# Kernel optimization log

Hardware: AMD Instinct MI355X
Metric: run time of the kernel (lower is better)

The kernel has to match this reference:

```python
import jax, jax.numpy as jnp
import numpy as np

B, N, C = 4, 1029, 1024
H = 16           # num_heads
L = 8            # num_blocks
DH = C // H      # head_dim = 64
HID = 4 * C      # mlp hidden
SCALE = DH ** -0.5
EPS = 1e-6


def _ln(x, w, b):
    mu = jnp.mean(x, axis=-1, keepdims=True)
    var = jnp.var(x, axis=-1, keepdims=True)
    return (x - mu) * jax.lax.rsqrt(var + EPS) * w + b


def setup_inputs() -> dict:
    key = jax.random.key(0)
    ks = jax.random.split(key, 16)
    s = 0.02
    return {
        "x": jax.random.normal(ks[0], (B, N, C), dtype=jnp.float32),
        "ln1_w": jnp.ones((L, C), jnp.float32),
        "ln1_b": jnp.zeros((L, C), jnp.float32),
        "qkv_w": jax.random.normal(ks[1], (L, 3 * C, C), jnp.float32) * s,
        "qkv_b": jnp.zeros((L, 3 * C), jnp.float32),
        "proj_w": jax.random.normal(ks[2], (L, C, C), jnp.float32) * s,
        "proj_b": jnp.zeros((L, C), jnp.float32),
        "ln2_w": jnp.ones((L, C), jnp.float32),
        "ln2_b": jnp.zeros((L, C), jnp.float32),
        "fc1_w": jax.random.normal(ks[3], (L, HID, C), jnp.float32) * s,
        "fc1_b": jnp.zeros((L, HID), jnp.float32),
        "fc2_w": jax.random.normal(ks[4], (L, C, HID), jnp.float32) * s,
        "fc2_b": jnp.zeros((L, C), jnp.float32),
        "norm_w": jnp.ones((C,), jnp.float32),
        "norm_b": jnp.zeros((C,), jnp.float32),
    }


def _block(x, p):
    ln1_w, ln1_b, qkv_w, qkv_b, proj_w, proj_b, ln2_w, ln2_b, fc1_w, fc1_b, fc2_w, fc2_b = p
    # --- attention (manual fp32 QK^T / softmax / AV, as in Attention.forward) ---
    h = _ln(x, ln1_w, ln1_b)
    qkv = h @ qkv_w.T + qkv_b                        # [B,N,3C]
    qkv = qkv.reshape(B, N, 3, H, DH).transpose(2, 0, 3, 1, 4)  # [3,B,H,N,DH]
    q, k, v = qkv[0], qkv[1], qkv[2]
    attn = jnp.einsum("bhnd,bhmd->bhnm", q.astype(jnp.float32), k.astype(jnp.float32)) * SCALE
    # original subtracts row max before softmax; jax.nn.softmax is the same stable math
    attn = jax.nn.softmax(attn, axis=-1).astype(v.dtype)
    o = jnp.einsum("bhnm,bhmd->bhnd", attn, v)       # [B,H,N,DH]
    o = o.transpose(0, 2, 1, 3).reshape(B, N, C)
    x = x + (o @ proj_w.T + proj_b)
    # --- MLP (exact GELU, as nn.GELU default) ---
    h = _ln(x, ln2_w, ln2_b)
    h = jax.nn.gelu(h @ fc1_w.T + fc1_b, approximate=False)
    x = x + (h @ fc2_w.T + fc2_b)
    return x


def reference(x, ln1_w, ln1_b, qkv_w, qkv_b, proj_w, proj_b, ln2_w, ln2_b,
              fc1_w, fc1_b, fc2_w, fc2_b, norm_w, norm_b):
    params = (ln1_w, ln1_b, qkv_w, qkv_b, proj_w, proj_b, ln2_w, ln2_b,
              fc1_w, fc1_b, fc2_w, fc2_b)

    def body(h, p):
        return _block(h, p), None

    x, _ = jax.lax.scan(body, x, params)
    return _ln(x, norm_w, norm_b)
```

## Files before the change

kernel.cpp:

```cpp
#include <hip/hip_runtime.h>
#include <cstdint>
#include <cstddef>

#define B_    4
#define N_TOK 1029
#define C_    1024
#define H_    16
#define DH_   64
#define L_    8
#define HID_  4096
#define M_TOK (B_*N_TOK)
#define MP2_  4352
#define GMB_  34
#define KVB_  128
#define KVT2_ 9
#define KPAD_ 1152

typedef float f32x4 __attribute__((ext_vector_type(4)));
typedef short bf16x8 __attribute__((ext_vector_type(8)));

__device__ __forceinline__ uint16_t f2bf(float f) {
  uint32_t u = __float_as_uint(f);
  u += 0x7fffu + ((u >> 16) & 1u);
  return (uint16_t)(u >> 16);
}

__device__ __forceinline__ void async_copy16(const uint16_t* src, uint16_t* lds_dst) {
  __builtin_amdgcn_global_load_lds(
      (const __attribute__((address_space(1))) void*)src,
      (__attribute__((address_space(3))) void*)lds_dst, 16, 0, 0);
}

__device__ __forceinline__ int swz16(int row, int byte_in_row) {
  return row * 128 + (byte_in_row ^ ((row & 7) << 4));
}


__global__ __launch_bounds__(256)
void cvt_packB(const float* __restrict__ in, uint16_t* __restrict__ out,
               int K, int logsteps, int matsize) {
  const int lyr = blockIdx.y;
  const int t = blockIdx.x * 256 + threadIdx.x;
  const int lane = t & 63;
  const int j = (t >> 6) & 3;
  const int kk = (t >> 8) & ((1 << logsteps) - 1);
  const int pn = t >> (8 + logsteps);
  const int n = pn * 64 + j * 16 + (lane & 15);
  const int k0 = (kk << 5) + (lane >> 4) * 8;
  const float* src = in + (size_t)lyr * matsize + (size_t)n * K + k0;
  const float4 v0 = *(const float4*)(src);
  const float4 v1 = *(const float4*)(src + 4);
  uint64_t p0 = (uint64_t)f2bf(v0.x) | ((uint64_t)f2bf(v0.y) << 16)
              | ((uint64_t)f2bf(v0.z) << 32) | ((uint64_t)f2bf(v0.w) << 48);
  uint64_t p1 = (uint64_t)f2bf(v1.x) | ((uint64_t)f2bf(v1.y) << 16)
              | ((uint64_t)f2bf(v1.z) << 32) | ((uint64_t)f2bf(v1.w) << 48);
  uint64_t* dst = (uint64_t*)(out + (size_t)lyr * matsize + (size_t)t * 8);
  dst[0] = p0; dst[1] = p1;
}

template<int OUTMODE>
__global__ __launch_bounds__(256)
void ln_fwd(const float* __restrict__ x, const float* __restrict__ w,
            const float* __restrict__ b, void* __restrict__ outp) {
  const int row = blockIdx.x;
  const int tid = threadIdx.x;
  const float4 v = reinterpret_cast<const float4*>(x + (size_t)row * C_)[tid];
  float s  = v.x + v.y + v.z + v.w;
  float s2 = v.x*v.x + v.y*v.y + v.z*v.z + v.w*v.w;
  #pragma unroll
  for (int d = 1; d < 64; d <<= 1) {
    s  += __shfl_xor(s, d);
    s2 += __shfl_xor(s2, d);
  }
  __shared__ float red[8];
  const int wv = tid >> 6;
  if ((tid & 63) == 0) { red[wv] = s; red[wv + 4] = s2; }
  __syncthreads();
  s  = red[0] + red[1] + red[2] + red[3];
  s2 = red[4] + red[5] + red[6] + red[7];
  const float mu = s * (1.0f / C_);
  const float rs = rsqrtf(fmaxf(s2 * (1.0f / C_) - mu * mu, 0.0f) + 1e-6f);
  const float4 wv4 = reinterpret_cast<const float4*>(w)[tid];
  const float4 bv4 = reinterpret_cast<const float4*>(b)[tid];
  const float o0 = (v.x - mu) * rs * wv4.x + bv4.x;
  const float o1 = (v.y - mu) * rs * wv4.y + bv4.y;
  const float o2 = (v.z - mu) * rs * wv4.z + bv4.z;
  const float o3 = (v.w - mu) * rs * wv4.w + bv4.w;
  if (OUTMODE == 2) {
    const int c0 = tid * 4;
    const int kk = c0 >> 5, l4p = (c0 >> 3) & 3, e0 = c0 & 7;
    const int pm = row >> 6, ii = (row >> 4) & 3;
    const int lanep = l4p * 16 + (row & 15);
    const uint64_t pk = (uint64_t)f2bf(o0) | ((uint64_t)f2bf(o1) << 16)
                      | ((uint64_t)f2bf(o2) << 32) | ((uint64_t)f2bf(o3) << 48);
    uint16_t* op = (uint16_t*)outp;
    *(uint64_t*)(op + ((((size_t)pm * 32 + kk) * 4 + ii) * 64 + lanep) * 8 + e0) = pk;
  } else {
    float4 o; o.x = o0; o.y = o1; o.z = o2; o.w = o3;
    reinterpret_cast<float4*>((float*)outp + (size_t)row * C_)[tid] = o;
  }
}

template<int EPI, int SPLIT>
__global__ __launch_bounds__(256, 3)
void gemm_reg(const uint16_t* __restrict__ Apk, const uint16_t* __restrict__ Bpk,
              const float* __restrict__ bias, uint16_t* __restrict__ outb,
              float* __restrict__ pbuf, int Nn, int K, int outKsteps,
              uint16_t* __restrict__ Qp, uint16_t* __restrict__ Kp,
              uint16_t* __restrict__ VTp) {
  const int nwg = (int)gridDim.x;
  const int q8 = nwg >> 3, r8 = nwg & 7;
  const int xcd = (int)blockIdx.x & 7, pos = (int)blockIdx.x >> 3;
  const int wgid = (xcd < r8 ? xcd * (q8 + 1) : r8 * (q8 + 1) + (xcd - r8) * q8) + pos;
  const int NB = Nn >> 7;
  const int kc  = (SPLIT > 1) ? wgid / (GMB_ * NB) : 0;
  const int rem = (SPLIT > 1) ? wgid % (GMB_ * NB) : wgid;
  const int bn = rem / GMB_, bm = rem % GMB_;

  const int tid = (int)threadIdx.x;
  const int l = tid & 63, w = tid >> 6;
  const int l15 = l & 15, l4 = l >> 4;
  const int wr = w >> 1, wc = w & 1;
  const int steps = K >> 5;
  const int kcsteps = steps / SPLIT;

  const uint16_t* Aw = Apk + ((size_t)(bm * 2 + wr) * steps + (size_t)kc * kcsteps) * 2048 + l * 8;
  const uint16_t* Bw = Bpk + ((size_t)(bn * 2 + wc) * steps + (size_t)kc * kcsteps) * 2048 + l * 8;

  f32x4 acc[4][4] = {};
  bf16x8 a0[4], b0[4], a1[4], b1[4];

  auto ld0 = [&](int s) {
    const uint16_t* ap = Aw + (size_t)s * 2048;
    const uint16_t* bp = Bw + (size_t)s * 2048;
    #pragma unroll
    for (int i = 0; i < 4; ++i) a0[i] = *(const bf16x8*)(ap + i * 512);
    #pragma unroll
    for (int j = 0; j < 4; ++j) b0[j] = *(const bf16x8*)(bp + j * 512);
  };
  auto ld1 = [&](int s) {
    const uint16_t* ap = Aw + (size_t)s * 2048;
    const uint16_t* bp = Bw + (size_t)s * 2048;
    #pragma unroll
    for (int i = 0; i < 4; ++i) a1[i] = *(const bf16x8*)(ap + i * 512);
    #pragma unroll
    for (int j = 0; j < 4; ++j) b1[j] = *(const bf16x8*)(bp + j * 512);
  };
  auto mm0 = [&] {
    #pragma unroll
    for (int i = 0; i < 4; ++i)
      #pragma unroll
      for (int j = 0; j < 4; ++j)
        acc[i][j] = __builtin_amdgcn_mfma_f32_16x16x32_bf16(a0[i], b0[j], acc[i][j], 0, 0, 0);
  };
  auto mm1 = [&] {
    #pragma unroll
    for (int i = 0; i < 4; ++i)
      #pragma unroll
      for (int j = 0; j < 4; ++j)
        acc[i][j] = __builtin_amdgcn_mfma_f32_16x16x32_bf16(a1[i], b1[j], acc[i][j], 0, 0, 0);
  };

  ld0(0);
  for (int s = 0; s + 2 <= kcsteps; s += 2) {
    ld1(s + 1);
    mm0();
    if (s + 2 < kcsteps) ld0(s + 2);
    mm1();
  }

  #pragma unroll
  for (int j = 0; j < 4; ++j) {
    const int col = bn * 128 + wc * 64 + j * 16 + l15;
    const float bv = (EPI == 3) ? 0.0f : bias[col];
    #pragma unroll
    for (int i = 0; i < 4; ++i) {
      const int mb = bm * 128 + wr * 64 + i * 16 + l4 * 4;
      #pragma unroll
      for (int r = 0; r < 4; ++r) {
        const int m = mb + r;
        const float v = acc[i][j][r] + bv;
        if (EPI == 1) {
          const float u = -1.5957691216f * (v + 0.044715f * v * v * v);
          const float g = v * __builtin_amdgcn_rcpf(1.0f + __expf(u));
          const int pm = m >> 6, ii = (m >> 4) & 3;
          const int kk = col >> 5, l4p = (col >> 3) & 3, e = col & 7;
          const int lanep = l4p * 16 + (m & 15);
          outb[((((size_t)pm * outKsteps + kk) * 4 + ii) * 64 + lanep) * 8 + e] = f2bf(g);
        } else if (EPI == 3) {
          pbuf[((size_t)kc * MP2_ + m) * C_ + col] = v;
        } else {
          if (m < M_TOK) {
            const int which = col >> 10;
            const int h = (col >> 6) & 15;
            const int d = col & 63;
            const int b = m / N_TOK;
            const int key = m - b * N_TOK;
            const int bh = b * 16 + h;
            if (which == 0)      Qp[((size_t)bh * KPAD_ + key) * 64 + d] = f2bf(v * 0.125f);
            else if (which == 1) Kp[((size_t)bh * KPAD_ + key) * 64 + d] = f2bf(v);
            else                 VTp[((size_t)bh * 64 + d) * KPAD_ + key] = f2bf(v);
          }
        }
      }
    }
  }
}

template<int KCH>
__global__ __launch_bounds__(256)
void reduce_add(const float* __restrict__ pbuf, const float* __restrict__ bias,
                float* __restrict__ xbuf) {
  const int m = blockIdx.x;
  const int c4 = threadIdx.x;
  float4 s = reinterpret_cast<const float4*>(bias)[c4];
  #pragma unroll
  for (int kc = 0; kc < KCH; ++kc) {
    const float4 pv = reinterpret_cast<const float4*>(pbuf + ((size_t)kc * MP2_ + m) * C_)[c4];
    s.x += pv.x; s.y += pv.y; s.z += pv.z; s.w += pv.w;
  }
  float4 x = reinterpret_cast<float4*>(xbuf + (size_t)m * C_)[c4];
  x.x += s.x; x.y += s.y; x.z += s.z; x.w += s.w;
  reinterpret_cast<float4*>(xbuf + (size_t)m * C_)[c4] = x;
}

__global__ __launch_bounds__(256, 3)
void attn_fwd(const uint16_t* __restrict__ Qp, const uint16_t* __restrict__ Kp,
              const uint16_t* __restrict__ VTp, uint16_t* __restrict__ ob) {
  __shared__ uint16_t Ksm_[KVB_ * 64];
  __shared__ uint16_t Vsm_[64 * KVB_];
  __shared__ uint16_t Psm_[4][16 * 136];

  const int tid = (int)threadIdx.x;
  const int l = tid & 63, w = tid >> 6;
  const int l15 = l & 15, l4 = l >> 4;
  const int bh = (int)blockIdx.x;
  const int qt = (int)blockIdx.y;

  const uint16_t* Kb = Kp + (size_t)bh * KPAD_ * 64;
  const uint16_t* Vb = VTp + (size_t)bh * 64 * KPAD_;

  bf16x8 qf[2];
  {
    const int qrow = qt * 64 + w * 16 + l15;
    const uint16_t* qbase = Qp + ((size_t)bh * KPAD_ + qrow) * 64;
    qf[0] = *(const bf16x8*)(qbase + l4 * 8);
    qf[1] = *(const bf16x8*)(qbase + 32 + l4 * 8);
  }

  float mrow = -1e30f, lrow = 0.0f;
  f32x4 oacc[4] = {};

  const int krow_s = tid >> 3;
  const int kslot_s = (tid & 7) ^ (krow_s & 7);
  const int vd_s = tid >> 4;
  const int vslot_s = (tid & 15) ^ (vd_s & 15);

  for (int kt = 0; kt < KVT2_; ++kt) {
    const int key0 = kt * KVB_;
    __syncthreads();
    #pragma unroll
    for (int it = 0; it < 4; ++it) {
      const int row = it * 32 + krow_s;
      async_copy16(Kb + (size_t)(key0 + row) * 64 + kslot_s * 8,
                   Ksm_ + it * 2048 + tid * 8);
    }
    #pragma unroll
    for (int it = 0; it < 4; ++it) {
      const int d = it * 16 + vd_s;
      async_copy16(Vb + (size_t)d * KPAD_ + key0 + vslot_s * 8,
                   Vsm_ + it * 2048 + tid * 8);
    }
    __syncthreads();

    f32x4 s[8];
    #pragma unroll
    for (int kf = 0; kf < 8; ++kf) s[kf] = f32x4{0.f, 0.f, 0.f, 0.f};
    #pragma unroll
    for (int kk = 0; kk < 2; ++kk) {
      #pragma unroll
      for (int kf = 0; kf < 8; ++kf) {
        const bf16x8 kfrag = *(const bf16x8*)((const char*)Ksm_ + swz16(kf * 16 + l15, kk * 64 + l4 * 16));
        s[kf] = __builtin_amdgcn_mfma_f32_16x16x32_bf16(kfrag, qf[kk], s[kf], 0, 0, 0);
      }
    }
    if (kt == KVT2_ - 1) {
      #pragma unroll
      for (int kf = 0; kf < 8; ++kf)
        #pragma unroll
        for (int r = 0; r < 4; ++r)
          if (key0 + kf * 16 + l4 * 4 + r >= N_TOK) s[kf][r] = -1e30f;
    }
    float pmx = s[0][0];
    #pragma unroll
    for (int kf = 0; kf < 8; ++kf)
      #pragma unroll
      for (int r = 0; r < 4; ++r) pmx = fmaxf(pmx, s[kf][r]);
    pmx = fmaxf(pmx, __shfl_xor(pmx, 16));
    pmx = fmaxf(pmx, __shfl_xor(pmx, 32));
    if (!__all(pmx - mrow <= 8.0f)) {
      const float mi = fmaxf(mrow, pmx);
      const float sc = __expf(mrow - mi);
      mrow = mi;
      lrow *= sc;
      #pragma unroll
      for (int df = 0; df < 4; ++df)
        #pragma unroll
        for (int r = 0; r < 4; ++r) oacc[df][r] *= sc;
    }
    float psum = 0.0f;
    #pragma unroll
    for (int kf = 0; kf < 8; ++kf) {
      const float p0 = __expf(s[kf][0] - mrow);
      const float p1 = __expf(s[kf][1] - mrow);
      const float p2 = __expf(s[kf][2] - mrow);
      const float p3 = __expf(s[kf][3] - mrow);
      psum += (p0 + p1) + (p2 + p3);
      const uint64_t pk = (uint64_t)f2bf(p0) | ((uint64_t)f2bf(p1) << 16)
                        | ((uint64_t)f2bf(p2) << 32) | ((uint64_t)f2bf(p3) << 48);
      *(uint64_t*)(&Psm_[w][l15 * 136 + kf * 16 + l4 * 4]) = pk;
    }
    psum += __shfl_xor(psum, 16);
    psum += __shfl_xor(psum, 32);
    lrow += psum;
    #pragma unroll
    for (int kk = 0; kk < 4; ++kk) {
      const bf16x8 pf = *(const bf16x8*)(&Psm_[w][l15 * 136 + kk * 32 + l4 * 8]);
      #pragma unroll
      for (int df = 0; df < 4; ++df) {
        const int d = df * 16 + l15;
        const bf16x8 vfrag = *(const bf16x8*)(Vsm_ + d * KVB_ + (((kk * 4 + l4) ^ (d & 15)) * 8));
        oacc[df] = __builtin_amdgcn_mfma_f32_16x16x32_bf16(vfrag, pf, oacc[df], 0, 0, 0);
      }
    }
  }

  const int q = qt * 64 + w * 16 + l15;
  if (q < N_TOK) {
    const float inv = 1.0f / lrow;
    const int m = (bh >> 4) * N_TOK + q;
    const int pmq = m >> 6, ii = (m >> 4) & 3, m15 = m & 15;
    const int hbase = (bh & 15) * 64;
    #pragma unroll
    for (int df = 0; df < 4; ++df)
      #pragma unroll
      for (int r = 0; r < 4; ++r) {
        const int c = hbase + df * 16 + l4 * 4 + r;
        const int kkp = c >> 5, l4p = (c >> 3) & 3, e = c & 7;
        ob[((((size_t)pmq * 32 + kkp) * 4 + ii) * 64 + l4p * 16 + m15) * 8 + e] =
            f2bf(oacc[df][r] * inv);
      }
  }
}

extern "C" void kernel_launch(void* const* d_in, const int* in_sizes, int n_in,
                              void* d_out, int out_size, void* d_ws, size_t ws_size,
                              hipStream_t stream) {
  const float* x_in   = (const float*)d_in[0];
  const float* ln1_w  = (const float*)d_in[1];
  const float* ln1_b  = (const float*)d_in[2];
  const float* qkv_w  = (const float*)d_in[3];
  const float* qkv_b  = (const float*)d_in[4];
  const float* proj_w = (const float*)d_in[5];
  const float* proj_b = (const float*)d_in[6];
  const float* ln2_w  = (const float*)d_in[7];
  const float* ln2_b  = (const float*)d_in[8];
  const float* fc1_w  = (const float*)d_in[9];
  const float* fc1_b  = (const float*)d_in[10];
  const float* fc2_w  = (const float*)d_in[11];
  const float* fc2_b  = (const float*)d_in[12];
  const float* norm_w = (const float*)d_in[13];
  const float* norm_b = (const float*)d_in[14];

  char* p = (char*)d_ws;
  float*    xbuf = (float*)p;     p += (size_t)MP2_ * C_ * 4;
  uint16_t* hbuf = (uint16_t*)p;  p += (size_t)MP2_ * C_ * 2;
  uint16_t* big  = (uint16_t*)p;  p += (size_t)MP2_ * HID_ * 2;
  uint16_t* wq   = (uint16_t*)p;  p += (size_t)L_ * 3 * C_ * C_ * 2;
  uint16_t* wp   = (uint16_t*)p;  p += (size_t)L_ * C_ * C_ * 2;
  uint16_t* w1   = (uint16_t*)p;  p += (size_t)L_ * HID_ * C_ * 2;
  uint16_t* w2   = (uint16_t*)p;  p += (size_t)L_ * C_ * HID_ * 2;
  uint16_t* qp   = (uint16_t*)p;  p += (size_t)64 * KPAD_ * 64 * 2;
  uint16_t* kp   = (uint16_t*)p;  p += (size_t)64 * KPAD_ * 64 * 2;
  uint16_t* vtp  = (uint16_t*)p;  p += (size_t)64 * 64 * KPAD_ * 2;
  float*    pbuf = (float*)p;     p += (size_t)2 * MP2_ * C_ * 4;
  if ((size_t)(p - (char*)d_ws) > ws_size) return;

  hipMemcpyAsync(xbuf, x_in, (size_t)M_TOK * C_ * sizeof(float),
                 hipMemcpyDeviceToDevice, stream);

  cvt_packB<<<dim3(3 * C_ * C_ / 2048, L_), dim3(256), 0, stream>>>(qkv_w,  wq, C_,   5, 3 * C_ * C_);
  cvt_packB<<<dim3(C_ * C_ / 2048, L_),     dim3(256), 0, stream>>>(proj_w, wp, C_,   5, C_ * C_);
  cvt_packB<<<dim3(HID_ * C_ / 2048, L_),   dim3(256), 0, stream>>>(fc1_w,  w1, C_,   5, HID_ * C_);
  cvt_packB<<<dim3(C_ * HID_ / 2048, L_),   dim3(256), 0, stream>>>(fc2_w,  w2, HID_, 7, C_ * HID_);

  for (int lyr = 0; lyr < L_; ++lyr) {
    ln_fwd<2><<<dim3(M_TOK), dim3(256), 0, stream>>>(
        xbuf, ln1_w + (size_t)lyr * C_, ln1_b + (size_t)lyr * C_, hbuf);
    gemm_reg<4, 1><<<dim3((3 * C_ / 128) * GMB_), dim3(256), 0, stream>>>(
        hbuf, wq + (size_t)lyr * 3 * C_ * C_, qkv_b + (size_t)lyr * 3 * C_,
        nullptr, nullptr, 3 * C_, C_, 0, qp, kp, vtp);
    attn_fwd<<<dim3(64, 17), dim3(256), 0, stream>>>(qp, kp, vtp, hbuf);
    gemm_reg<3, 2><<<dim3(2 * (C_ / 128) * GMB_), dim3(256), 0, stream>>>(
        hbuf, wp + (size_t)lyr * C_ * C_, nullptr,
        nullptr, pbuf, C_, C_, 0, nullptr, nullptr, nullptr);
    reduce_add<2><<<dim3(M_TOK), dim3(256), 0, stream>>>(
        pbuf, proj_b + (size_t)lyr * C_, xbuf);
    ln_fwd<2><<<dim3(M_TOK), dim3(256), 0, stream>>>(
        xbuf, ln2_w + (size_t)lyr * C_, ln2_b + (size_t)lyr * C_, hbuf);
    gemm_reg<1, 1><<<dim3((HID_ / 128) * GMB_), dim3(256), 0, stream>>>(
        hbuf, w1 + (size_t)lyr * HID_ * C_, fc1_b + (size_t)lyr * HID_,
        big, nullptr, HID_, C_, HID_ >> 5, nullptr, nullptr, nullptr);
    gemm_reg<3, 2><<<dim3(2 * (C_ / 128) * GMB_), dim3(256), 0, stream>>>(
        big, w2 + (size_t)lyr * C_ * HID_, nullptr,
        nullptr, pbuf, C_, HID_, 0, nullptr, nullptr, nullptr);
    reduce_add<2><<<dim3(M_TOK), dim3(256), 0, stream>>>(
        pbuf, fc2_b + (size_t)lyr * C_, xbuf);
  }
  ln_fwd<1><<<dim3(M_TOK), dim3(256), 0, stream>>>(xbuf, norm_w, norm_b, d_out);
}
```

Baseline: 2.795 ms.

## Replace register-direct packed GEMM with LDS double-buffered 256x256 tile GEMM

Swaps the old GEMM, which loaded pre-packed bf16 fragments straight into registers, for a 512-thread kernel. The new kernel stages 256x256 tiles of row-major A and W into swizzled LDS with async global-to-LDS copies and double buffering. A separate 256-thread tail path handles the leftover rows beyond 4096. The packed layouts are dropped: weights are converted with a plain elementwise cast, and LN and attention write row-major bf16. The fc2 split-K goes from 2 to 4, which adds reduction traffic in exchange for more workgroups. The larger tiles raise data reuse per workgroup but cut the workgroup count and occupancy, and the tail path is a simple unpipelined loop.

```diff
diff --git a/kernel.cpp b/kernel.cpp
--- a/kernel.cpp
+++ b/kernel.cpp
@@ -6,12 +6,12 @@
 #define N_TOK 1029
 #define C_    1024
 #define H_    16
-#define DH_   64
 #define L_    8
 #define HID_  4096
 #define M_TOK (B_*N_TOK)
 #define MP2_  4352
-#define GMB_  34
+#define TM0_  4096
+#define PROWS 4224
 #define KVB_  128
 #define KVT2_ 9
 #define KPAD_ 1152
@@ -35,27 +35,15 @@
   return row * 128 + (byte_in_row ^ ((row & 7) << 4));
 }
 
-
 __global__ __launch_bounds__(256)
-void cvt_packB(const float* __restrict__ in, uint16_t* __restrict__ out,
-               int K, int logsteps, int matsize) {
-  const int lyr = blockIdx.y;
-  const int t = blockIdx.x * 256 + threadIdx.x;
-  const int lane = t & 63;
-  const int j = (t >> 6) & 3;
-  const int kk = (t >> 8) & ((1 << logsteps) - 1);
-  const int pn = t >> (8 + logsteps);
-  const int n = pn * 64 + j * 16 + (lane & 15);
-  const int k0 = (kk << 5) + (lane >> 4) * 8;
-  const float* src = in + (size_t)lyr * matsize + (size_t)n * K + k0;
-  const float4 v0 = *(const float4*)(src);
-  const float4 v1 = *(const float4*)(src + 4);
-  uint64_t p0 = (uint64_t)f2bf(v0.x) | ((uint64_t)f2bf(v0.y) << 16)
-              | ((uint64_t)f2bf(v0.z) << 32) | ((uint64_t)f2bf(v0.w) << 48);
-  uint64_t p1 = (uint64_t)f2bf(v1.x) | ((uint64_t)f2bf(v1.y) << 16)
-              | ((uint64_t)f2bf(v1.z) << 32) | ((uint64_t)f2bf(v1.w) << 48);
-  uint64_t* dst = (uint64_t*)(out + (size_t)lyr * matsize + (size_t)t * 8);
-  dst[0] = p0; dst[1] = p1;
+void cvt_f32_bf16(const float* __restrict__ in, uint16_t* __restrict__ out, int n4) {
+  int i = blockIdx.x * 256 + threadIdx.x;
+  if (i < n4) {
+    float4 v = reinterpret_cast<const float4*>(in)[i];
+    uint64_t pk = (uint64_t)f2bf(v.x) | ((uint64_t)f2bf(v.y) << 16)
+                | ((uint64_t)f2bf(v.z) << 32) | ((uint64_t)f2bf(v.w) << 48);
+    reinterpret_cast<uint64_t*>(out)[i] = pk;
+  }
 }
 
 template<int OUTMODE>
@@ -86,123 +74,196 @@
   const float o1 = (v.y - mu) * rs * wv4.y + bv4.y;
   const float o2 = (v.z - mu) * rs * wv4.z + bv4.z;
   const float o3 = (v.w - mu) * rs * wv4.w + bv4.w;
-  if (OUTMODE == 2) {
-    const int c0 = tid * 4;
-    const int kk = c0 >> 5, l4p = (c0 >> 3) & 3, e0 = c0 & 7;
-    const int pm = row >> 6, ii = (row >> 4) & 3;
-    const int lanep = l4p * 16 + (row & 15);
-    const uint64_t pk = (uint64_t)f2bf(o0) | ((uint64_t)f2bf(o1) << 16)
-                      | ((uint64_t)f2bf(o2) << 32) | ((uint64_t)f2bf(o3) << 48);
-    uint16_t* op = (uint16_t*)outp;
-    *(uint64_t*)(op + ((((size_t)pm * 32 + kk) * 4 + ii) * 64 + lanep) * 8 + e0) = pk;
+  if (OUTMODE == 0) {
+    uint64_t pk = (uint64_t)f2bf(o0) | ((uint64_t)f2bf(o1) << 16)
+                | ((uint64_t)f2bf(o2) << 32) | ((uint64_t)f2bf(o3) << 48);
+    reinterpret_cast<uint64_t*>((uint16_t*)outp + (size_t)row * C_)[tid] = pk;
   } else {
     float4 o; o.x = o0; o.y = o1; o.z = o2; o.w = o3;
     reinterpret_cast<float4*>((float*)outp + (size_t)row * C_)[tid] = o;
   }
 }
 
+template<int EPI>
+__device__ __forceinline__ void epi_store(int m, int col, float v, int Nn, int kc,
+    const float* bias, uint16_t* outb, float* pbuf,
+    uint16_t* Qp, uint16_t* Kp, uint16_t* VTp) {
+  if (EPI == 3) {
+    pbuf[((size_t)kc * PROWS + m) * Nn + col] = v;
+  } else if (EPI == 1) {
+    const float vb = v + bias[col];
+    const float u = -1.5957691216f * (vb + 0.044715f * vb * vb * vb);
+    const float g = vb * __builtin_amdgcn_rcpf(1.0f + __expf(u));
+    outb[(size_t)m * Nn + col] = f2bf(g);
+  } else {
+    if (m < M_TOK) {
+      const float vb = v + bias[col];
+      const int which = col >> 10;
+      const int h = (col >> 6) & 15;
+      const int d = col & 63;
+      const int b = m / N_TOK;
+      const int key = m - b * N_TOK;
+      const int bh = b * 16 + h;
+      if (which == 0)      Qp[((size_t)bh * KPAD_ + key) * 64 + d] = f2bf(vb * 0.125f);
+      else if (which == 1) Kp[((size_t)bh * KPAD_ + key) * 64 + d] = f2bf(vb);
+      else                 VTp[((size_t)bh * 64 + d) * KPAD_ + key] = f2bf(vb);
+    }
+  }
+}
+
 template<int EPI, int SPLIT>
-__global__ __launch_bounds__(256, 3)
-void gemm_reg(const uint16_t* __restrict__ Apk, const uint16_t* __restrict__ Bpk,
-              const float* __restrict__ bias, uint16_t* __restrict__ outb,
-              float* __restrict__ pbuf, int Nn, int K, int outKsteps,
-              uint16_t* __restrict__ Qp, uint16_t* __restrict__ Kp,
-              uint16_t* __restrict__ VTp) {
+__global__ __launch_bounds__(512)
+void gemm8p(const uint16_t* __restrict__ A, const uint16_t* __restrict__ W,
+            const float* __restrict__ bias, uint16_t* __restrict__ outb,
+            float* __restrict__ pbuf,
+            uint16_t* __restrict__ Qp, uint16_t* __restrict__ Kp,
+            uint16_t* __restrict__ VTp, int Nn, int Ktot) {
+  const int nbn = Nn >> 8;
+  const int MAIN = 16 * nbn * SPLIT;
+  const int KC = Ktot / SPLIT;
   const int nwg = (int)gridDim.x;
   const int q8 = nwg >> 3, r8 = nwg & 7;
   const int xcd = (int)blockIdx.x & 7, pos = (int)blockIdx.x >> 3;
   const int wgid = (xcd < r8 ? xcd * (q8 + 1) : r8 * (q8 + 1) + (xcd - r8) * q8) + pos;
-  const int NB = Nn >> 7;
-  const int kc  = (SPLIT > 1) ? wgid / (GMB_ * NB) : 0;
-  const int rem = (SPLIT > 1) ? wgid % (GMB_ * NB) : wgid;
-  const int bn = rem / GMB_, bm = rem % GMB_;
-
   const int tid = (int)threadIdx.x;
+
+  if (wgid >= MAIN) {
+    if (tid >= 256) return;
+    const int tailid = wgid - MAIN;
+    const int tnb = Nn >> 7;
+    const int tbn = tailid % tnb, tkc = tailid / tnb;
+    const int l = tid & 63, w2 = tid >> 6;
+    const int l15 = l & 15, l4 = l >> 4;
+    const int wr = w2 >> 1, wc = w2 & 1;
+    const uint16_t* Ag = A + (size_t)(TM0_ + wr * 64) * Ktot + (size_t)tkc * KC;
+    const uint16_t* Wg = W + (size_t)(tbn * 128 + wc * 64) * Ktot + (size_t)tkc * KC;
+    f32x4 acc[4][4] = {};
+    const int ks = KC >> 5;
+    for (int s = 0; s < ks; ++s) {
+      bf16x8 af[4], bf[4];
+      #pragma unroll
+      for (int i = 0; i < 4; ++i)
+        af[i] = *(const bf16x8*)(Ag + (size_t)(i * 16 + l15) * Ktot + s * 32 + l4 * 8);
+      #pragma unroll
+      for (int j = 0; j < 4; ++j)
+        bf[j] = *(const bf16x8*)(Wg + (size_t)(j * 16 + l15) * Ktot + s * 32 + l4 * 8);
+      #pragma unroll
+      for (int i = 0; i < 4; ++i)
+        #pragma unroll
+        for (int j = 0; j < 4; ++j)
+          acc[i][j] = __builtin_amdgcn_mfma_f32_16x16x32_bf16(af[i], bf[j], acc[i][j], 0, 0, 0);
+    }
+    #pragma unroll
+    for (int j = 0; j < 4; ++j) {
+      const int col = tbn * 128 + wc * 64 + j * 16 + l15;
+      #pragma unroll
+      for (int i = 0; i < 4; ++i) {
+        #pragma unroll
+        for (int r = 0; r < 4; ++r) {
+          const int m = TM0_ + wr * 64 + i * 16 + l4 * 4 + r;
+          epi_store<EPI>(m, col, acc[i][j][r], Nn, tkc, bias, outb, pbuf, Qp, Kp, VTp);
+        }
+      }
+    }
+    return;
+  }
+
+  __shared__ char lds[131072];
+  const int kc  = (SPLIT > 1) ? wgid / (16 * nbn) : 0;
+  const int rem = (SPLIT > 1) ? wgid % (16 * nbn) : wgid;
+  const int bm = rem & 15, bn = rem >> 4;
   const int l = tid & 63, w = tid >> 6;
   const int l15 = l & 15, l4 = l >> 4;
-  const int wr = w >> 1, wc = w & 1;
-  const int steps = K >> 5;
-  const int kcsteps = steps / SPLIT;
-
-  const uint16_t* Aw = Apk + ((size_t)(bm * 2 + wr) * steps + (size_t)kc * kcsteps) * 2048 + l * 8;
-  const uint16_t* Bw = Bpk + ((size_t)(bn * 2 + wc) * steps + (size_t)kc * kcsteps) * 2048 + l * 8;
-
-  f32x4 acc[4][4] = {};
-  bf16x8 a0[4], b0[4], a1[4], b1[4];
-
-  auto ld0 = [&](int s) {
-    const uint16_t* ap = Aw + (size_t)s * 2048;
-    const uint16_t* bp = Bw + (size_t)s * 2048;
-    #pragma unroll
-    for (int i = 0; i < 4; ++i) a0[i] = *(const bf16x8*)(ap + i * 512);
-    #pragma unroll
-    for (int j = 0; j < 4; ++j) b0[j] = *(const bf16x8*)(bp + j * 512);
+  const int wr = w >> 2, wc = w & 3;
+
+  const uint16_t* Ag = A + (size_t)bm * 256 * Ktot + (size_t)kc * KC;
+  const uint16_t* Wg = W + (size_t)bn * 256 * Ktot + (size_t)kc * KC;
+
+  const int srow = tid >> 3;
+  const int schunk = (tid & 7) ^ (srow & 7);
+  auto stage = [&](int mat, int j, int toff, int pdst) {
+    const int rbase = mat ? (j * 64) : ((j & 1) * 128 + ((j >> 1)) * 64);
+    const uint16_t* src = (mat ? Wg : Ag)
+        + (size_t)(rbase + srow) * Ktot + toff + schunk * 8;
+    uint16_t* dst = (uint16_t*)(lds + pdst * 65536 + mat * 32768 + rbase * 128 + tid * 16);
+    async_copy16(src, dst);
   };
-  auto ld1 = [&](int s) {
-    const uint16_t* ap = Aw + (size_t)s * 2048;
-    const uint16_t* bp = Bw + (size_t)s * 2048;
-    #pragma unroll
-    for (int i = 0; i < 4; ++i) a1[i] = *(const bf16x8*)(ap + i * 512);
-    #pragma unroll
-    for (int j = 0; j < 4; ++j) b1[j] = *(const bf16x8*)(bp + j * 512);
-  };
-  auto mm0 = [&] {
-    #pragma unroll
-    for (int i = 0; i < 4; ++i)
-      #pragma unroll
-      for (int j = 0; j < 4; ++j)
-        acc[i][j] = __builtin_amdgcn_mfma_f32_16x16x32_bf16(a0[i], b0[j], acc[i][j], 0, 0, 0);
-  };
-  auto mm1 = [&] {
-    #pragma unroll
-    for (int i = 0; i < 4; ++i)
-      #pragma unroll
-      for (int j = 0; j < 4; ++j)
-        acc[i][j] = __builtin_amdgcn_mfma_f32_16x16x32_bf16(a1[i], b1[j], acc[i][j], 0, 0, 0);
-  };
-
-  ld0(0);
-  for (int s = 0; s + 2 <= kcsteps; s += 2) {
-    ld1(s + 1);
-    mm0();
-    if (s + 2 < kcsteps) ld0(s + 2);
-    mm1();
+
+  const int csel0 = ((l4) ^ (l15 & 7)) * 16;
+  const int csel1 = ((4 + l4) ^ (l15 & 7)) * 16;
+
+  f32x4 acc[8][4] = {};
+  stage(1, 0, 0, 0); stage(1, 1, 0, 0); stage(1, 2, 0, 0); stage(1, 3, 0, 0);
+  stage(0, 0, 0, 0); stage(0, 1, 0, 0); stage(0, 2, 0, 0); stage(0, 3, 0, 0);
+
+  const int nt = KC >> 6;
+  bf16x8 bfr[2][4];
+  for (int t = 0; t < nt; ++t) {
+    const int p = t & 1;
+    const char* base = lds + p * 65536;
+    const int toff = (t + 1) * 64;
+    const bool more = (t + 1 < nt);
+    asm volatile("s_waitcnt vmcnt(2)" ::: "memory");
+    __builtin_amdgcn_sched_barrier(0);
+    __builtin_amdgcn_s_barrier();
+    bf16x8 afr[4][2];
+    #pragma unroll
+    for (int f = 0; f < 4; ++f) {
+      const int rb = (wr * 128 + f * 16 + l15) * 128;
+      afr[f][0] = *(const bf16x8*)(base + rb + csel0);
+      afr[f][1] = *(const bf16x8*)(base + rb + csel1);
+    }
+    #pragma unroll
+    for (int nf = 0; nf < 4; ++nf) {
+      const int rb = 32768 + (wc * 64 + nf * 16 + l15) * 128;
+      bfr[0][nf] = *(const bf16x8*)(base + rb + csel0);
+      bfr[1][nf] = *(const bf16x8*)(base + rb + csel1);
+    }
+    if (more) {
+      stage(1, 0, toff, p ^ 1); stage(1, 1, toff, p ^ 1);
+      stage(1, 2, toff, p ^ 1); stage(1, 3, toff, p ^ 1);
+      stage(0, 0, toff, p ^ 1); stage(0, 1, toff, p ^ 1);
+    }
+    __builtin_amdgcn_s_setprio(1);
+    #pragma unroll
+    for (int kk = 0; kk < 2; ++kk)
+      #pragma unroll
+      for (int f = 0; f < 4; ++f)
+        #pragma unroll
+        for (int nf = 0; nf < 4; ++nf)
+          acc[f][nf] = __builtin_amdgcn_mfma_f32_16x16x32_bf16(afr[f][kk], bfr[kk][nf], acc[f][nf], 0, 0, 0);
+    __builtin_amdgcn_s_setprio(0);
+    if (t == nt - 1) asm volatile("s_waitcnt vmcnt(0)" ::: "memory");
+    else             asm volatile("s_waitcnt vmcnt(6)" ::: "memory");
+    __builtin_amdgcn_sched_barrier(0);
+    __builtin_amdgcn_s_barrier();
+    #pragma unroll
+    for (int f = 0; f < 4; ++f) {
+      const int rb = (wr * 128 + 64 + f * 16 + l15) * 128;
+      afr[f][0] = *(const bf16x8*)(base + rb + csel0);
+      afr[f][1] = *(const bf16x8*)(base + rb + csel1);
+    }
+    if (more) { stage(0, 2, toff, p ^ 1); stage(0, 3, toff, p ^ 1); }
+    __builtin_amdgcn_s_setprio(1);
+    #pragma unroll
+    for (int kk = 0; kk < 2; ++kk)
+      #pragma unroll
+      for (int f = 0; f < 4; ++f)
+        #pragma unroll
+        for (int nf = 0; nf < 4; ++nf)
+          acc[4 + f][nf] = __builtin_amdgcn_mfma_f32_16x16x32_bf16(afr[f][kk], bfr[kk][nf], acc[4 + f][nf], 0, 0, 0);
+    __builtin_amdgcn_s_setprio(0);
   }
 
   #pragma unroll
-  for (int j = 0; j < 4; ++j) {
-    const int col = bn * 128 + wc * 64 + j * 16 + l15;
-    const float bv = (EPI == 3) ? 0.0f : bias[col];
-    #pragma unroll
-    for (int i = 0; i < 4; ++i) {
-      const int mb = bm * 128 + wr * 64 + i * 16 + l4 * 4;
-      #pragma unroll
-      for (int r = 0; r < 4; ++r) {
-        const int m = mb + r;
-        const float v = acc[i][j][r] + bv;
-        if (EPI == 1) {
-          const float u = -1.5957691216f * (v + 0.044715f * v * v * v);
-          const float g = v * __builtin_amdgcn_rcpf(1.0f + __expf(u));
-          const int pm = m >> 6, ii = (m >> 4) & 3;
-          const int kk = col >> 5, l4p = (col >> 3) & 3, e = col & 7;
-          const int lanep = l4p * 16 + (m & 15);
-          outb[((((size_t)pm * outKsteps + kk) * 4 + ii) * 64 + lanep) * 8 + e] = f2bf(g);
-        } else if (EPI == 3) {
-          pbuf[((size_t)kc * MP2_ + m) * C_ + col] = v;
-        } else {
-          if (m < M_TOK) {
-            const int which = col >> 10;
-            const int h = (col >> 6) & 15;
-            const int d = col & 63;
-            const int b = m / N_TOK;
-            const int key = m - b * N_TOK;
-            const int bh = b * 16 + h;
-            if (which == 0)      Qp[((size_t)bh * KPAD_ + key) * 64 + d] = f2bf(v * 0.125f);
-            else if (which == 1) Kp[((size_t)bh * KPAD_ + key) * 64 + d] = f2bf(v);
-            else                 VTp[((size_t)bh * 64 + d) * KPAD_ + key] = f2bf(v);
-          }
-        }
-      }
+  for (int nf = 0; nf < 4; ++nf) {
+    const int col = bn * 256 + wc * 64 + nf * 16 + l15;
+    #pragma unroll
+    for (int mf = 0; mf < 8; ++mf) {
+      const int mb = bm * 256 + wr * 128 + mf * 16 + l4 * 4;
+      #pragma unroll
+      for (int r = 0; r < 4; ++r)
+        epi_store<EPI>(mb + r, col, acc[mf][nf][r], Nn, kc, bias, outb, pbuf, Qp, Kp, VTp);
     }
   }
 }
@@ -216,7 +277,7 @@
   float4 s = reinterpret_cast<const float4*>(bias)[c4];
   #pragma unroll
   for (int kc = 0; kc < KCH; ++kc) {
-    const float4 pv = reinterpret_cast<const float4*>(pbuf + ((size_t)kc * MP2_ + m) * C_)[c4];
+    const float4 pv = reinterpret_cast<const float4*>(pbuf + ((size_t)kc * PROWS + m) * C_)[c4];
     s.x += pv.x; s.y += pv.y; s.z += pv.z; s.w += pv.w;
   }
   float4 x = reinterpret_cast<float4*>(xbuf + (size_t)m * C_)[c4];
@@ -339,16 +400,13 @@
   if (q < N_TOK) {
     const float inv = 1.0f / lrow;
     const int m = (bh >> 4) * N_TOK + q;
-    const int pmq = m >> 6, ii = (m >> 4) & 3, m15 = m & 15;
     const int hbase = (bh & 15) * 64;
     #pragma unroll
     for (int df = 0; df < 4; ++df)
       #pragma unroll
       for (int r = 0; r < 4; ++r) {
         const int c = hbase + df * 16 + l4 * 4 + r;
-        const int kkp = c >> 5, l4p = (c >> 3) & 3, e = c & 7;
-        ob[((((size_t)pmq * 32 + kkp) * 4 + ii) * 64 + l4p * 16 + m15) * 8 + e] =
-            f2bf(oacc[df][r] * inv);
+        ob[(size_t)m * C_ + c] = f2bf(oacc[df][r] * inv);
       }
   }
 }
@@ -383,38 +441,42 @@
   uint16_t* qp   = (uint16_t*)p;  p += (size_t)64 * KPAD_ * 64 * 2;
   uint16_t* kp   = (uint16_t*)p;  p += (size_t)64 * KPAD_ * 64 * 2;
   uint16_t* vtp  = (uint16_t*)p;  p += (size_t)64 * 64 * KPAD_ * 2;
-  float*    pbuf = (float*)p;     p += (size_t)2 * MP2_ * C_ * 4;
+  float*    pbuf = (float*)p;     p += (size_t)4 * PROWS * C_ * 4;
   if ((size_t)(p - (char*)d_ws) > ws_size) return;
 
   hipMemcpyAsync(xbuf, x_in, (size_t)M_TOK * C_ * sizeof(float),
                  hipMemcpyDeviceToDevice, stream);
 
-  cvt_packB<<<dim3(3 * C_ * C_ / 2048, L_), dim3(256), 0, stream>>>(qkv_w,  wq, C_,   5, 3 * C_ * C_);
-  cvt_packB<<<dim3(C_ * C_ / 2048, L_),     dim3(256), 0, stream>>>(proj_w, wp, C_,   5, C_ * C_);
-  cvt_packB<<<dim3(HID_ * C_ / 2048, L_),   dim3(256), 0, stream>>>(fc1_w,  w1, C_,   5, HID_ * C_);
-  cvt_packB<<<dim3(C_ * HID_ / 2048, L_),   dim3(256), 0, stream>>>(fc2_w,  w2, HID_, 7, C_ * HID_);
+  auto cvt = [&](const float* src, uint16_t* dst, size_t n) {
+    const int n4 = (int)(n / 4);
+    cvt_f32_bf16<<<dim3((n4 + 255) / 256), dim3(256), 0, stream>>>(src, dst, n4);
+  };
+  cvt(qkv_w,  wq, (size_t)L_ * 3 * C_ * C_);
+  cvt(proj_w, wp, (size_t)L_ * C_ * C_);
+  cvt(fc1_w,  w1, (size_t)L_ * HID_ * C_);
+  cvt(fc2_w,  w2, (size_t)L_ * C_ * HID_);
 
   for (int lyr = 0; lyr < L_; ++lyr) {
-    ln_fwd<2><<<dim3(M_TOK), dim3(256), 0, stream>>>(
+    ln_fwd<0><<<dim3(M_TOK), dim3(256), 0, stream>>>(
         xbuf, ln1_w + (size_t)lyr * C_, ln1_b + (size_t)lyr * C_, hbuf);
-    gemm_reg<4, 1><<<dim3((3 * C_ / 128) * GMB_), dim3(256), 0, stream>>>(
+    gemm8p<0, 1><<<dim3(216), dim3(512), 0, stream>>>(
         hbuf, wq + (size_t)lyr * 3 * C_ * C_, qkv_b + (size_t)lyr * 3 * C_,
-        nullptr, nullptr, 3 * C_, C_, 0, qp, kp, vtp);
+        nullptr, nullptr, qp, kp, vtp, 3 * C_, C_);
     attn_fwd<<<dim3(64, 17), dim3(256), 0, stream>>>(qp, kp, vtp, hbuf);
-    gemm_reg<3, 2><<<dim3(2 * (C_ / 128) * GMB_), dim3(256), 0, stream>>>(
+    gemm8p<3, 2><<<dim3(144), dim3(512), 0, stream>>>(
         hbuf, wp + (size_t)lyr * C_ * C_, nullptr,
-        nullptr, pbuf, C_, C_, 0, nullptr, nullptr, nullptr);
+        nullptr, pbuf, nullptr, nullptr, nullptr, C_, C_);
     reduce_add<2><<<dim3(M_TOK), dim3(256), 0, stream>>>(
         pbuf, proj_b + (size_t)lyr * C_, xbuf);
-    ln_fwd<2><<<dim3(M_TOK), dim3(256), 0, stream>>>(
+    ln_fwd<0><<<dim3(M_TOK), dim3(256), 0, stream>>>(
         xbuf, ln2_w + (size_t)lyr * C_, ln2_b + (size_t)lyr * C_, hbuf);
-    gemm_reg<1, 1><<<dim3((HID_ / 128) * GMB_), dim3(256), 0, stream>>>(
+    gemm8p<1, 1><<<dim3(288), dim3(512), 0, stream>>>(
         hbuf, w1 + (size_t)lyr * HID_ * C_, fc1_b + (size_t)lyr * HID_,
-        big, nullptr, HID_, C_, HID_ >> 5, nullptr, nullptr, nullptr);
-    gemm_reg<3, 2><<<dim3(2 * (C_ / 128) * GMB_), dim3(256), 0, stream>>>(
+        big, nullptr, nullptr, nullptr, nullptr, HID_, C_);
+    gemm8p<3, 4><<<dim3(288), dim3(512), 0, stream>>>(
         big, w2 + (size_t)lyr * C_ * HID_, nullptr,
-        nullptr, pbuf, C_, HID_, 0, nullptr, nullptr, nullptr);
-    reduce_add<2><<<dim3(M_TOK), dim3(256), 0, stream>>>(
+        nullptr, pbuf, nullptr, nullptr, nullptr, C_, HID_);
+    reduce_add<4><<<dim3(M_TOK), dim3(256), 0, stream>>>(
         pbuf, fc2_b + (size_t)lyr * C_, xbuf);
   }
   ln_fwd<1><<<dim3(M_TOK), dim3(256), 0, stream>>>(xbuf, norm_w, norm_b, d_out);
```

New measurement: 2.770 ms. Within noise of the previous version (-0.9%).
